# Optimization experiments

Hardware: AMD Instinct MI355X
Metric: run time of the kernel (lower is better)

The kernel has to match this reference:

```python
import jax, jax.numpy as jnp
import numpy as np


def setup_inputs() -> dict:
    key = jax.random.key(0)
    k1, k2, k3 = jax.random.split(key, 3)
    B, N, K, F, H = 4, 50000, 10, 128, 16
    x = jax.random.normal(k1, (B, N, K, F), dtype=jnp.float32)
    # xavier-like scales for learned params
    W = jax.random.normal(k2, (F, 4 * H), dtype=jnp.float32) * (1.0 / np.sqrt(F))
    a = jax.random.normal(k3, (4, H), dtype=jnp.float32) * 0.5
    return {"x": x, "W": W, "a": a}


def reference(x, W, a):
    # x: [B, N, K, F]; W: [F, 4H] (head-major blocks of 4); a: [4, H]
    B, N, K, F = x.shape
    H = a.shape[1]
    Wr = W.reshape(F, H, 4)                              # per-head projection
    hw = jnp.einsum('bnkf,fhd->bnkhd', x, Wr)            # [B,N,K,H,4]
    logits = jnp.einsum('bnkhd,dh->bnkh', hw, a)         # [B,N,K,H]
    attn = jax.nn.softmax(logits, axis=2)                # softmax over K neighbors
    out = jnp.einsum('bnkh,bnkhd->bnhd', attn, hw)       # [B,N,H,4]
    out = jax.nn.leaky_relu(out, negative_slope=0.2)
    out = out.reshape(B, N, H * 4)                       # concat over heads
    return out.transpose(0, 2, 1)                        # [B, 4H, N]
```

## Files before the change

### kernel.cpp

```cpp
#include <hip/hip_runtime.h>

typedef short bf16x8 __attribute__((ext_vector_type(8)));
typedef float f32x4 __attribute__((ext_vector_type(4)));

constexpr int Bc = 4;
constexpr int Nc = 50000;
constexpr int Kc = 10;
constexpr int Fc = 128;
constexpr int Hc = 16;
constexpr int Cc = 64;
constexpr int NODES = Bc * Nc;
constexpr int NPB = 8;
constexpr int ROWS = NPB * Kc;
constexpr int MT = ROWS / 16;
constexpr int BLK = 256;

constexpr int LDS_BYTES = 23936;
constexpr int OL_OFF = 21760;

__device__ __forceinline__ unsigned short f2bf(float f) {
    unsigned u = __builtin_bit_cast(unsigned, f);
    return (unsigned short)((u + 0x7fffu + ((u >> 16) & 1u)) >> 16);
}

__global__ __launch_bounds__(256)
void prep_w(const float* __restrict__ W, unsigned short* __restrict__ wt) {
    const int dst = blockIdx.x * 256 + threadIdx.x;
    const int j  = dst & 7;
    const int kc = (dst >> 3) & 3;
    const int l  = (dst >> 5) & 63;
    const int w  = dst >> 11;
    const int c  = w * 16 + (l & 15);
    const int f  = kc * 32 + (l >> 4) * 8 + j;
    wt[dst] = f2bf(W[f * 64 + c]);
}

__global__ __launch_bounds__(BLK, 6)
void gat_kernel(const float* __restrict__ x,
                const unsigned short* __restrict__ wt_ws,
                const float* __restrict__ a,
                float* __restrict__ out)
{
    __shared__ __align__(16) char smem[LDS_BYTES];

    const int t  = threadIdx.x;
    const int w  = t >> 6;
    const int l  = t & 63;
    const int lr = l & 15;
    const int lk = l >> 4;

    bf16x8 bfrag[4];
    {
        const bf16x8* wp = reinterpret_cast<const bf16x8*>(wt_ws + w * 2048 + l * 32);
#pragma unroll
        for (int kc = 0; kc < 4; ++kc) bfrag[kc] = wp[kc];
    }

    {
        const float* xg = x + (size_t)blockIdx.x * (ROWS * Fc);
#pragma unroll
        for (int i = 0; i < 5; ++i) {
            const int e0 = i * 2048 + t * 8;
            const float4 v0 = *reinterpret_cast<const float4*>(xg + e0);
            const float4 v1 = *reinterpret_cast<const float4*>(xg + e0 + 4);
            const int row = i * 16 + (t >> 4);
            const int byt = ((t & 15) * 16) ^ ((row & 7) << 4);
            uint4 p;
            p.x = (unsigned)f2bf(v0.x) | ((unsigned)f2bf(v0.y) << 16);
            p.y = (unsigned)f2bf(v0.z) | ((unsigned)f2bf(v0.w) << 16);
            p.z = (unsigned)f2bf(v1.x) | ((unsigned)f2bf(v1.y) << 16);
            p.w = (unsigned)f2bf(v1.z) | ((unsigned)f2bf(v1.w) << 16);
            *reinterpret_cast<uint4*>(smem + row * 256 + byt) = p;
        }
    }
    __syncthreads();

    f32x4 acc[MT];
#pragma unroll
    for (int m = 0; m < MT; ++m) acc[m] = (f32x4){0.f, 0.f, 0.f, 0.f};

#pragma unroll
    for (int m = 0; m < MT; ++m) {
        const int row = m * 16 + lr;
        const char* xrow = smem + row * 256;
        const int sw = (row & 7) << 4;
#pragma unroll
        for (int kc = 0; kc < 4; ++kc) {
            const bf16x8 af = *reinterpret_cast<const bf16x8*>(xrow + ((kc * 64 + lk * 16) ^ sw));
            acc[m] = __builtin_amdgcn_mfma_f32_16x16x32_bf16(af, bfrag[kc], acc[m], 0, 0, 0);
        }
    }
    __syncthreads();

    {
        float* hw = reinterpret_cast<float*>(smem);
        const int col = w * 16 + lr;
#pragma unroll
        for (int m = 0; m < MT; ++m) {
            const int rbase = m * 16 + lk * 4;
#pragma unroll
            for (int r = 0; r < 4; ++r)
                hw[(rbase + r) * 68 + col] = acc[m][r];
        }
    }
    __syncthreads();

    const float* hw = reinterpret_cast<const float*>(smem);
    float* ol = reinterpret_cast<float*>(smem + OL_OFF);
    if (t < NPB * Hc) {
        const int h  = t & 15;
        const int ln = t >> 4;
        const float ar0 = a[0 * Hc + h];
        const float ar1 = a[1 * Hc + h];
        const float ar2 = a[2 * Hc + h];
        const float ar3 = a[3 * Hc + h];

        float4 hv[Kc];
        float  lg[Kc];
        float  mx = -1e30f;
#pragma unroll
        for (int k = 0; k < Kc; ++k) {
            hv[k] = *reinterpret_cast<const float4*>(hw + (ln * Kc + k) * 68 + h * 4);
            lg[k] = fmaf(hv[k].x, ar0, fmaf(hv[k].y, ar1, fmaf(hv[k].z, ar2, hv[k].w * ar3)));
            mx = fmaxf(mx, lg[k]);
        }
        float lsum = 0.f, o0 = 0.f, o1 = 0.f, o2 = 0.f, o3 = 0.f;
#pragma unroll
        for (int k = 0; k < Kc; ++k) {
            const float p = __expf(lg[k] - mx);
            lsum += p;
            o0 = fmaf(p, hv[k].x, o0);
            o1 = fmaf(p, hv[k].y, o1);
            o2 = fmaf(p, hv[k].z, o2);
            o3 = fmaf(p, hv[k].w, o3);
        }
        const float inv = 1.f / lsum;
        o0 *= inv; o1 *= inv; o2 *= inv; o3 *= inv;
        o0 = fmaxf(o0, 0.2f * o0);
        o1 = fmaxf(o1, 0.2f * o1);
        o2 = fmaxf(o2, 0.2f * o2);
        o3 = fmaxf(o3, 0.2f * o3);
        *reinterpret_cast<float4*>(ol + ln * 68 + h * 4) = make_float4(o0, o1, o2, o3);
    }
    __syncthreads();

    if (t < 128) {
        const int c  = t >> 1;
        const int nq = t & 1;
        const int nb = blockIdx.x * NPB;
        const int b  = nb / Nc;
        const int n0 = nb - b * Nc;
        float4 v;
        v.x = ol[(nq * 4 + 0) * 68 + c];
        v.y = ol[(nq * 4 + 1) * 68 + c];
        v.z = ol[(nq * 4 + 2) * 68 + c];
        v.w = ol[(nq * 4 + 3) * 68 + c];
        *reinterpret_cast<float4*>(out + ((size_t)b * Cc + c) * Nc + n0 + nq * 4) = v;
    }
}

extern "C" void kernel_launch(void* const* d_in, const int* in_sizes, int n_in,
                              void* d_out, int out_size, void* d_ws, size_t ws_size,
                              hipStream_t stream) {
    const float* x = (const float*)d_in[0];
    const float* W = (const float*)d_in[1];
    const float* a = (const float*)d_in[2];
    float* out = (float*)d_out;
    unsigned short* wt = (unsigned short*)d_ws;

    prep_w<<<32, 256, 0, stream>>>(W, wt);
    gat_kernel<<<NODES / NPB, BLK, 0, stream>>>(x, wt, a, out);
}
```

Measured before the change: 235.9 us.

## Use packed bf16 convert, online softmax, tighter LDS and higher occupancy

```diff
diff --git a/kernel.cpp b/kernel.cpp
--- a/kernel.cpp
+++ b/kernel.cpp
@@ -14,13 +14,20 @@
 constexpr int ROWS = NPB * Kc;
 constexpr int MT = ROWS / 16;
 constexpr int BLK = 256;
+constexpr int NTILES = NODES / NPB;
 
-constexpr int LDS_BYTES = 23936;
-constexpr int OL_OFF = 21760;
+constexpr int OL_OFF = 20480;
+constexpr int LDS_BYTES = 22528;
 
 __device__ __forceinline__ unsigned short f2bf(float f) {
     unsigned u = __builtin_bit_cast(unsigned, f);
     return (unsigned short)((u + 0x7fffu + ((u >> 16) & 1u)) >> 16);
+}
+
+__device__ __forceinline__ unsigned cvtpk(float lo, float hi) {
+    unsigned r;
+    asm("v_cvt_pk_bf16_f32 %0, %1, %2" : "=v"(r) : "v"(lo), "v"(hi));
+    return r;
 }
 
 __global__ __launch_bounds__(256)
@@ -35,7 +42,7 @@
     wt[dst] = f2bf(W[f * 64 + c]);
 }
 
-__global__ __launch_bounds__(BLK, 6)
+__global__ __launch_bounds__(BLK, 8)
 void gat_kernel(const float* __restrict__ x,
                 const unsigned short* __restrict__ wt_ws,
                 const float* __restrict__ a,
@@ -49,41 +56,39 @@
     const int lr = l & 15;
     const int lk = l >> 4;
 
+    {
+        const float* xg = x + (size_t)blockIdx.x * (ROWS * Fc);
+        const int r0 = t >> 4;
+        const int sw = (r0 & 7) << 4;
+        char* wr = smem + r0 * 256 + (((t & 15) * 16) ^ sw);
+#pragma unroll 1
+        for (int i = 0; i < 5; ++i) {
+            const float4 v0 = *reinterpret_cast<const float4*>(xg + i * 2048 + t * 8);
+            const float4 v1 = *reinterpret_cast<const float4*>(xg + i * 2048 + t * 8 + 4);
+            uint4 p;
+            p.x = cvtpk(v0.x, v0.y);
+            p.y = cvtpk(v0.z, v0.w);
+            p.z = cvtpk(v1.x, v1.y);
+            p.w = cvtpk(v1.z, v1.w);
+            *reinterpret_cast<uint4*>(wr + i * 4096) = p;
+        }
+    }
+
     bf16x8 bfrag[4];
     {
         const bf16x8* wp = reinterpret_cast<const bf16x8*>(wt_ws + w * 2048 + l * 32);
 #pragma unroll
         for (int kc = 0; kc < 4; ++kc) bfrag[kc] = wp[kc];
     }
-
-    {
-        const float* xg = x + (size_t)blockIdx.x * (ROWS * Fc);
-#pragma unroll
-        for (int i = 0; i < 5; ++i) {
-            const int e0 = i * 2048 + t * 8;
-            const float4 v0 = *reinterpret_cast<const float4*>(xg + e0);
-            const float4 v1 = *reinterpret_cast<const float4*>(xg + e0 + 4);
-            const int row = i * 16 + (t >> 4);
-            const int byt = ((t & 15) * 16) ^ ((row & 7) << 4);
-            uint4 p;
-            p.x = (unsigned)f2bf(v0.x) | ((unsigned)f2bf(v0.y) << 16);
-            p.y = (unsigned)f2bf(v0.z) | ((unsigned)f2bf(v0.w) << 16);
-            p.z = (unsigned)f2bf(v1.x) | ((unsigned)f2bf(v1.y) << 16);
-            p.w = (unsigned)f2bf(v1.z) | ((unsigned)f2bf(v1.w) << 16);
-            *reinterpret_cast<uint4*>(smem + row * 256 + byt) = p;
-        }
-    }
     __syncthreads();
 
     f32x4 acc[MT];
 #pragma unroll
     for (int m = 0; m < MT; ++m) acc[m] = (f32x4){0.f, 0.f, 0.f, 0.f};
-
 #pragma unroll
     for (int m = 0; m < MT; ++m) {
-        const int row = m * 16 + lr;
-        const char* xrow = smem + row * 256;
-        const int sw = (row & 7) << 4;
+        const char* xrow = smem + (m * 16 + lr) * 256;
+        const int sw = (lr & 7) << 4;
 #pragma unroll
         for (int kc = 0; kc < 4; ++kc) {
             const bf16x8 af = *reinterpret_cast<const bf16x8*>(xrow + ((kc * 64 + lk * 16) ^ sw));
@@ -100,39 +105,35 @@
             const int rbase = m * 16 + lk * 4;
 #pragma unroll
             for (int r = 0; r < 4; ++r)
-                hw[(rbase + r) * 68 + col] = acc[m][r];
+                hw[(rbase + r) * 64 + col] = acc[m][r];
         }
     }
     __syncthreads();
 
-    const float* hw = reinterpret_cast<const float*>(smem);
-    float* ol = reinterpret_cast<float*>(smem + OL_OFF);
     if (t < NPB * Hc) {
         const int h  = t & 15;
         const int ln = t >> 4;
-        const float ar0 = a[0 * Hc + h];
-        const float ar1 = a[1 * Hc + h];
-        const float ar2 = a[2 * Hc + h];
-        const float ar3 = a[3 * Hc + h];
+        const float ar0 = a[h];
+        const float ar1 = a[16 + h];
+        const float ar2 = a[32 + h];
+        const float ar3 = a[48 + h];
+        const float* hwb = reinterpret_cast<const float*>(smem) + (ln * Kc) * 64 + h * 4;
 
-        float4 hv[Kc];
-        float  lg[Kc];
-        float  mx = -1e30f;
+        float mx = -1e30f, lsum = 0.f;
+        float o0 = 0.f, o1 = 0.f, o2 = 0.f, o3 = 0.f;
 #pragma unroll
         for (int k = 0; k < Kc; ++k) {
-            hv[k] = *reinterpret_cast<const float4*>(hw + (ln * Kc + k) * 68 + h * 4);
-            lg[k] = fmaf(hv[k].x, ar0, fmaf(hv[k].y, ar1, fmaf(hv[k].z, ar2, hv[k].w * ar3)));
-            mx = fmaxf(mx, lg[k]);
-        }
-        float lsum = 0.f, o0 = 0.f, o1 = 0.f, o2 = 0.f, o3 = 0.f;
-#pragma unroll
-        for (int k = 0; k < Kc; ++k) {
-            const float p = __expf(lg[k] - mx);
-            lsum += p;
-            o0 = fmaf(p, hv[k].x, o0);
-            o1 = fmaf(p, hv[k].y, o1);
-            o2 = fmaf(p, hv[k].z, o2);
-            o3 = fmaf(p, hv[k].w, o3);
+            const float4 hv = *reinterpret_cast<const float4*>(hwb + k * 64);
+            const float lg = fmaf(hv.x, ar0, fmaf(hv.y, ar1, fmaf(hv.z, ar2, hv.w * ar3)));
+            const float mn = fmaxf(mx, lg);
+            const float s  = __expf(mx - mn);
+            const float p  = __expf(lg - mn);
+            mx = mn;
+            lsum = fmaf(lsum, s, p);
+            o0 = fmaf(o0, s, p * hv.x);
+            o1 = fmaf(o1, s, p * hv.y);
+            o2 = fmaf(o2, s, p * hv.z);
+            o3 = fmaf(o3, s, p * hv.w);
         }
         const float inv = 1.f / lsum;
         o0 *= inv; o1 *= inv; o2 *= inv; o3 *= inv;
@@ -140,21 +141,23 @@
         o1 = fmaxf(o1, 0.2f * o1);
         o2 = fmaxf(o2, 0.2f * o2);
         o3 = fmaxf(o3, 0.2f * o3);
-        *reinterpret_cast<float4*>(ol + ln * 68 + h * 4) = make_float4(o0, o1, o2, o3);
+        float* ol = reinterpret_cast<float*>(smem + OL_OFF);
+        *reinterpret_cast<float4*>(ol + ln * 64 + h * 4) = make_float4(o0, o1, o2, o3);
     }
     __syncthreads();
 
     if (t < 128) {
+        const float* ol = reinterpret_cast<const float*>(smem + OL_OFF);
         const int c  = t >> 1;
         const int nq = t & 1;
         const int nb = blockIdx.x * NPB;
         const int b  = nb / Nc;
         const int n0 = nb - b * Nc;
         float4 v;
-        v.x = ol[(nq * 4 + 0) * 68 + c];
-        v.y = ol[(nq * 4 + 1) * 68 + c];
-        v.z = ol[(nq * 4 + 2) * 68 + c];
-        v.w = ol[(nq * 4 + 3) * 68 + c];
+        v.x = ol[(nq * 4 + 0) * 64 + c];
+        v.y = ol[(nq * 4 + 1) * 64 + c];
+        v.z = ol[(nq * 4 + 2) * 64 + c];
+        v.w = ol[(nq * 4 + 3) * 64 + c];
         *reinterpret_cast<float4*>(out + ((size_t)b * Cc + c) * Nc + n0 + nq * 4) = v;
     }
 }
@@ -169,5 +172,5 @@
     unsigned short* wt = (unsigned short*)d_ws;
 
     prep_w<<<32, 256, 0, stream>>>(W, wt);
-    gat_kernel<<<NODES / NPB, BLK, 0, stream>>>(x, wt, a, out);
+    gat_kernel<<<NTILES, BLK, 0, stream>>>(x, wt, a, out);
 }
```

Result: no change. 236.9 us (+0.4%).
